# Kernel optimization log

Hardware: AMD Instinct MI355X
Metric: run time of the kernel (lower is better)

Reference implementation:

```python
import jax, jax.numpy as jnp
import numpy as np

N_NODES = 100000
N_EDGES = 3200000
N_GRAPHS = 2048
D_IN = 128
D_H = 128
D_OUT = 2
BN_EPS = 1e-5


def setup_inputs() -> dict:
    key = jax.random.key(0)
    ks = jax.random.split(key, 24)
    x = jax.random.normal(ks[0], (N_NODES, D_IN), dtype=jnp.float32)
    edge_index = jax.random.randint(ks[1], (2, N_EDGES), 0, N_NODES, dtype=jnp.int64)
    batch = jnp.sort(jax.random.randint(ks[2], (N_NODES,), 0, N_GRAPHS, dtype=jnp.int64))

    def lin(k, din, dout):
        return jax.random.normal(k, (din, dout), dtype=jnp.float32) / np.sqrt(din)

    inp = {
        'x': x, 'edge_index': edge_index, 'batch': batch,
        'W1': lin(ks[3], D_IN, D_H), 'b1': jnp.zeros((D_H,), jnp.float32),
        'W2': lin(ks[4], D_H, D_H), 'b2': jnp.zeros((D_H,), jnp.float32),
        'W3': lin(ks[5], D_H, D_H), 'b3': jnp.zeros((D_H,), jnp.float32),
    }
    for i, kk in zip((1, 2, 3), (ks[6], ks[7], ks[8])):
        inp[f'bn{i}_g'] = 1.0 + 0.1 * jax.random.normal(jax.random.fold_in(kk, 0), (D_H,), jnp.float32)
        inp[f'bn{i}_b'] = 0.1 * jax.random.normal(jax.random.fold_in(kk, 1), (D_H,), jnp.float32)
        inp[f'bn{i}_m'] = 0.1 * jax.random.normal(jax.random.fold_in(kk, 2), (D_H,), jnp.float32)
        inp[f'bn{i}_v'] = 0.5 + jax.random.uniform(jax.random.fold_in(kk, 3), (D_H,), jnp.float32)
    inp['fc1_W'] = lin(ks[9], D_H, D_H)
    inp['fc1_b'] = jnp.zeros((D_H,), jnp.float32)
    inp['fc2_W'] = lin(ks[10], D_H, D_OUT)
    inp['fc2_b'] = jnp.zeros((D_OUT,), jnp.float32)
    return inp


def _gcn_conv(x, W, b, src, dst, dinv):
    # h = X W, then out[dst] += (dinv[src]*dinv[dst]) * h[src]  (self-loops already in src/dst)
    h = x @ W
    norm = dinv[src] * dinv[dst]  # [E+N]
    msg = h[src] * norm[:, None]  # [E+N, D]
    out = jax.ops.segment_sum(msg, dst, num_segments=N_NODES)
    return out + b


def _bn_eval(x, g, b, m, v):
    return (x - m) * (g * jax.lax.rsqrt(v + BN_EPS)) + b


def reference(x, edge_index, batch, W1, b1, W2, b2, W3, b3,
              bn1_g, bn1_b, bn1_m, bn1_v, bn2_g, bn2_b, bn2_m, bn2_v,
              bn3_g, bn3_b, bn3_m, bn3_v, fc1_W, fc1_b, fc2_W, fc2_b):
    loops = jnp.arange(N_NODES, dtype=edge_index.dtype)
    src = jnp.concatenate([edge_index[0], loops])
    dst = jnp.concatenate([edge_index[1], loops])
    deg = jax.ops.segment_sum(jnp.ones_like(dst, dtype=x.dtype), dst, num_segments=N_NODES)
    dinv = jnp.where(deg > 0, jax.lax.rsqrt(jnp.maximum(deg, 1.0)), 0.0)

    h = jax.nn.relu(_bn_eval(_gcn_conv(x, W1, b1, src, dst, dinv), bn1_g, bn1_b, bn1_m, bn1_v))
    h = jax.nn.relu(_bn_eval(_gcn_conv(h, W2, b2, src, dst, dinv), bn2_g, bn2_b, bn2_m, bn2_v))
    h = jax.nn.relu(_bn_eval(_gcn_conv(h, W3, b3, src, dst, dinv), bn3_g, bn3_b, bn3_m, bn3_v))

    # global mean pool over graphs
    sums = jax.ops.segment_sum(h, batch, num_segments=N_GRAPHS)
    cnts = jax.ops.segment_sum(jnp.ones((N_NODES,), h.dtype), batch, num_segments=N_GRAPHS)
    pooled = sums / jnp.maximum(cnts, 1.0)[:, None]  # [G, D_H]

    z = jax.nn.relu(pooled @ fc1_W + fc1_b)
    logits = z @ fc2_W + fc2_b
    return jax.nn.log_softmax(logits, axis=1)
```

## Files before the change

### kernel.cpp

```cpp
#include <hip/hip_runtime.h>
#include <stdint.h>

#define NN 100000
#define NE 3200000
#define NG 2048
#define DH 128
#define NBLK_SCAN 49

#define NBUK 196
#define BSH 9
#define BMASK 511
#define BUKCAP 18200
#define EPT 16
#define EPW 4096

typedef __attribute__((ext_vector_type(8))) short v8s;
typedef __attribute__((ext_vector_type(4))) float v4f;

__device__ __forceinline__ float bf2f(unsigned short u) {
  union { unsigned int i; float f; } v; v.i = ((unsigned int)u) << 16; return v.f;
}
__device__ __forceinline__ unsigned short f2bf(float f) {
  union { float f; unsigned int i; } v; v.f = f;
  unsigned int i = v.i;
  unsigned int r = (i + 0x7FFFu + ((i >> 16) & 1u)) >> 16;
  return (unsigned short)r;
}
__device__ __forceinline__ int eload(const void* p, long long i, int is64) {
  return is64 ? (int)((const long long*)p)[i] : ((const int*)p)[i];
}
__device__ __forceinline__ float pload(const void* p, int i, int isbf) {
  return isbf ? bf2f(((const unsigned short*)p)[i]) : ((const float*)p)[i];
}
__device__ __forceinline__ void upadd(unsigned int w, float& lo, float& hi) {
  union { unsigned int u; float f; } a, b;
  a.u = w << 16; b.u = w & 0xffff0000u;
  lo += a.f; hi += b.f;
}

constexpr size_t al(size_t x) { return (x + 255) & ~size_t(255); }
constexpr size_t OFF_FLAGS = 0;
constexpr size_t OFF_DINV  = 256;
constexpr size_t OFF_ROWP  = al(OFF_DINV + 4ull * NN);
constexpr size_t OFF_GSTART= al(OFF_ROWP + 4ull * (NN + 1));
constexpr size_t OFF_BCUR  = al(OFF_GSTART + 4ull * (NG + 1));
constexpr size_t OFF_BSUM  = al(OFF_BCUR + 1024);
constexpr size_t OFF_BPRE  = al(OFF_BSUM + 256);
constexpr size_t OFF_WT    = al(OFF_BPRE + 256);
constexpr size_t OFF_FC1W  = al(OFF_WT + 2ull * 3 * 16384);
constexpr size_t OFF_FC2W  = al(OFF_FC1W + 4ull * 16384);
constexpr size_t OFF_PVEC  = al(OFF_FC2W + 4ull * 256);
constexpr size_t OFF_AC    = al(OFF_PVEC + 4ull * 17 * 128);
constexpr size_t OFF_COL   = al(OFF_AC + 4ull * 768);
constexpr size_t OFF_H     = al(OFF_COL + 4ull * NE);
constexpr size_t OFF_Y     = al(OFF_H + 2ull * NN * 128);
constexpr size_t WS_NEED   = OFF_Y + 2ull * NN * 128;
constexpr size_t OFF_REC   = OFF_H;
constexpr size_t OFF_DEG   = WS_NEED - 4ull * NN;

__global__ __launch_bounds__(256) void zero_k(int* p, int n) {
  int i = blockIdx.x * 256 + threadIdx.x;
  if (i < n) p[i] = 0;
}

__global__ __launch_bounds__(256) void probe_k(const void* edge, const void* batch,
                                               const void* x, int* flags) {
  __shared__ int cnt_e, cnt_b, cnt_f;
  int t = threadIdx.x;
  if (t == 0) { cnt_e = 0; cnt_b = 0; cnt_f = 0; }
  __syncthreads();
  int le = 0, lb = 0, lf = 0;
  for (int i = t; i < 512; i += 256) {
    uint2 p = ((const uint2*)edge)[i + 64];
    if (p.y != 0) le++;
  }
  for (int i = t; i < 512; i += 256) {
    uint2 p = ((const uint2*)batch)[50000 - 512 + i];
    if (p.y != 0) lb++;
  }
  for (int i = t; i < 4096; i += 256) {
    unsigned short u = ((const unsigned short*)x)[i];
    int e = (u >> 7) & 0xFF;
    if (e >= 0x90) lf++;
  }
  atomicAdd(&cnt_e, le); atomicAdd(&cnt_b, lb); atomicAdd(&cnt_f, lf);
  __syncthreads();
  if (t == 0) {
    flags[0] = (cnt_e == 0);
    flags[1] = (cnt_b == 0);
    flags[2] = (cnt_f < 16);
    flags[3] = 1;
  }
}

struct Ptrs { const void* p[22]; };

__global__ __launch_bounds__(256) void norm_param_k(Ptrs ptrs, const int* flags,
    unsigned short* Wt, float* fc1W, float* fc2W, float* pvec) {
  int isbf = flags[2];
  int idx = blockIdx.x * 256 + threadIdx.x;
  if (idx < 3 * 16384) {
    int l = idx / 16384, rem = idx % 16384;
    int c = rem >> 7, k = rem & 127;
    const void* W = ptrs.p[2 * l];
    Wt[l * 16384 + c * DH + k] = f2bf(pload(W, k * DH + c, isbf));
  } else if (idx < 4 * 16384) {
    int jj = idx - 3 * 16384;
    fc1W[jj] = pload(ptrs.p[18], jj, isbf);
  } else if (idx < 4 * 16384 + 256) {
    int jj = idx - 4 * 16384;
    fc2W[jj] = pload(ptrs.p[20], jj, isbf);
  } else if (idx < 4 * 16384 + 256 + 17 * 128) {
    int jj = idx - (4 * 16384 + 256);
    int slot = jj >> 7, e = jj & 127;
    int pi = (slot < 3) ? (1 + 2 * slot) : (slot < 15) ? (slot + 3) : (slot == 15 ? 19 : 21);
    if (slot == 16 && e >= 2) return;
    pvec[slot * 128 + e] = pload(ptrs.p[pi], e, isbf);
  }
}

__global__ __launch_bounds__(256) void prep_k(const float* pvec, float* AC) {
  int idx = blockIdx.x * 256 + threadIdx.x;
  if (idx >= 384) return;
  int l = idx >> 7, d = idx & 127;
  float b  = pvec[l * 128 + d];
  float g  = pvec[(3 + 4 * l) * 128 + d];
  float bb = pvec[(4 + 4 * l) * 128 + d];
  float m  = pvec[(5 + 4 * l) * 128 + d];
  float v  = pvec[(6 + 4 * l) * 128 + d];
  float s = g * rsqrtf(v + 1e-5f);
  AC[l * 256 + d] = s;
  AC[l * 256 + 128 + d] = (b - m) * s + bb;
}

__global__ __launch_bounds__(256) void partition_k(const void* edge, const int* flags,
    int* bcur, unsigned long long* recs) {
  __shared__ int lhist[NBUK];
  __shared__ int lbase[NBUK];
  __shared__ int lrank[NBUK];
  int t = threadIdx.x;
  for (int b = t; b < NBUK; b += 256) { lhist[b] = 0; lrank[b] = 0; }
  __syncthreads();
  long long e0 = (long long)blockIdx.x * EPW;
  int f = flags[0];
  int sv[EPT], dv[EPT];
  #pragma unroll
  for (int k = 0; k < EPT; ++k) {
    long long e = e0 + k * 256 + t;
    int s = 0, d = -1;
    if (e < NE) {
      s = eload(edge, e, f);
      d = eload(edge, NE + e, f);
      if ((unsigned)s >= NN || (unsigned)d >= NN) d = -1;
    }
    sv[k] = s; dv[k] = d;
    if (d >= 0) atomicAdd(&lhist[d >> BSH], 1);
  }
  __syncthreads();
  for (int b = t; b < NBUK; b += 256)
    lbase[b] = atomicAdd(&bcur[b], lhist[b]);
  __syncthreads();
  #pragma unroll
  for (int k = 0; k < EPT; ++k) {
    int d = dv[k];
    if (d >= 0) {
      int b = d >> BSH;
      int r = atomicAdd(&lrank[b], 1);
      int pos = lbase[b] + r;
      if (pos < BUKCAP)
        recs[(size_t)b * BUKCAP + pos] =
            ((unsigned long long)(unsigned)d << 32) | (unsigned)sv[k];
    }
  }
}

__global__ __launch_bounds__(256) void bucket_deg_k(const unsigned long long* recs,
    const int* bcur, int* deg) {
  __shared__ int lh[1 << BSH];
  int b = blockIdx.x, t = threadIdx.x;
  for (int i = t; i < (1 << BSH); i += 256) lh[i] = 0;
  __syncthreads();
  int cnt = bcur[b]; if (cnt > BUKCAP) cnt = BUKCAP;
  const unsigned long long* rb = recs + (size_t)b * BUKCAP;
  for (int i = t; i < cnt; i += 256) {
    int d = (int)(rb[i] >> 32);
    atomicAdd(&lh[d & BMASK], 1);
  }
  __syncthreads();
  int base = b << BSH;
  for (int i = t; i < (1 << BSH); i += 256) {
    int n = base + i;
    if (n < NN) deg[n] = lh[i];
  }
}

__global__ __launch_bounds__(256) void debucket_k(const unsigned long long* recs,
    const int* bcur, const int* rowp, int* colv) {
  __shared__ int lrk[1 << BSH];
  int b = blockIdx.x, t = threadIdx.x;
  for (int i = t; i < (1 << BSH); i += 256) lrk[i] = 0;
  __syncthreads();
  int cnt = bcur[b]; if (cnt > BUKCAP) cnt = BUKCAP;
  const unsigned long long* rb = recs + (size_t)b * BUKCAP;
  for (int i = t; i < cnt; i += 256) {
    unsigned long long rec = rb[i];
    int d = (int)(rec >> 32);
    int s = (int)(rec & 0xffffffffu);
    int r = atomicAdd(&lrk[d & BMASK], 1);
    colv[rowp[d] + r] = s;
  }
}

__global__ __launch_bounds__(256) void dinv_k(const int* deg, float* dinv) {
  int n = blockIdx.x * 256 + threadIdx.x;
  if (n < NN) dinv[n] = rsqrtf((float)(deg[n] + 1));
}

__global__ __launch_bounds__(256) void scan1_k(const int* deg, int* bsum) {
  __shared__ int ts[256];
  int t = threadIdx.x;
  int base = blockIdx.x * 2048 + t * 8;
  int s = 0;
  #pragma unroll
  for (int k = 0; k < 8; ++k) { int i = base + k; s += (i < NN) ? deg[i] : 0; }
  ts[t] = s; __syncthreads();
  for (int off = 128; off > 0; off >>= 1) {
    if (t < off) ts[t] += ts[t + off];
    __syncthreads();
  }
  if (t == 0) bsum[blockIdx.x] = ts[0];
}

__global__ void scan2_k(const int* bsum, int* bpre, int* rowp) {
  if (threadIdx.x == 0 && blockIdx.x == 0) {
    int run = 0;
    for (int b = 0; b < NBLK_SCAN; ++b) { bpre[b] = run; run += bsum[b]; }
    rowp[NN] = run;
  }
}

__global__ __launch_bounds__(256) void scan3_k(const int* deg, const int* bpre, int* rowp) {
  __shared__ int ts[256];
  int t = threadIdx.x;
  int base = blockIdx.x * 2048 + t * 8;
  int v[8]; int s = 0;
  #pragma unroll
  for (int k = 0; k < 8; ++k) { int i = base + k; v[k] = (i < NN) ? deg[i] : 0; s += v[k]; }
  ts[t] = s; __syncthreads();
  for (int off = 1; off < 256; off <<= 1) {
    int x = (t >= off) ? ts[t - off] : 0;
    __syncthreads();
    ts[t] += x;
    __syncthreads();
  }
  int pre = bpre[blockIdx.x] + ts[t] - s;
  #pragma unroll
  for (int k = 0; k < 8; ++k) { int i = base + k; if (i < NN) rowp[i] = pre; pre += v[k]; }
}

__global__ __launch_bounds__(256) void gbound_k(const void* batch, const int* flags,
                                                int* gstart) {
  int i = blockIdx.x * 256 + threadIdx.x;
  if (i >= NN) return;
  int f = flags[1];
  int b = eload(batch, i, f);
  if ((unsigned)b >= NG) b = NG - 1;
  int bp = -1;
  if (i > 0) {
    bp = eload(batch, i - 1, f);
    if ((unsigned)bp >= NG) bp = NG - 1;
  }
  for (int g = bp + 1; g <= b; ++g) gstart[g] = i;
  if (i == NN - 1) {
    for (int g = b + 1; g <= NG; ++g) gstart[g] = NN;
  }
}

__global__ __launch_bounds__(256) void gemm_k(const void* A, const int* flagp,
    const unsigned short* Wt, const float* dinv, unsigned short* H) {
  const int wave = threadIdx.x >> 6;
  const int lane = threadIdx.x & 63;
  const int rowbase = blockIdx.x * 64 + wave * 16;
  const int r = lane & 15;
  const int g = lane >> 4;
  const int isb = flagp[0];
  int arow = rowbase + r;
  int arowc = (arow < NN) ? arow : 0;

  v8s a[4];
  if (isb) {
    const uint4* Ab = (const uint4*)A;
    #pragma unroll
    for (int ks = 0; ks < 4; ++ks) {
      union { uint4 u; v8s v; } t;
      t.u = Ab[(arowc * DH + ks * 32 + g * 8) >> 3];
      a[ks] = t.v;
    }
  } else {
    const float4* Af = (const float4*)A;
    #pragma unroll
    for (int ks = 0; ks < 4; ++ks) {
      int bi = (arowc * DH + ks * 32 + g * 8) >> 2;
      float4 f0 = Af[bi], f1 = Af[bi + 1];
      v8s t;
      t[0]=(short)f2bf(f0.x); t[1]=(short)f2bf(f0.y); t[2]=(short)f2bf(f0.z); t[3]=(short)f2bf(f0.w);
      t[4]=(short)f2bf(f1.x); t[5]=(short)f2bf(f1.y); t[6]=(short)f2bf(f1.z); t[7]=(short)f2bf(f1.w);
      a[ks] = t;
    }
  }
  int orow0 = rowbase + g * 4;
  float dv[4];
  #pragma unroll
  for (int j = 0; j < 4; ++j) {
    int orow = orow0 + j;
    dv[j] = dinv[(orow < NN) ? orow : 0];
  }
  const uint4* Wb = (const uint4*)Wt;
  #pragma unroll
  for (int ct = 0; ct < 8; ++ct) {
    v4f acc = {0.f, 0.f, 0.f, 0.f};
    #pragma unroll
    for (int ks = 0; ks < 4; ++ks) {
      union { uint4 u; v8s v; } t;
      t.u = Wb[((ct * 16 + r) * DH + ks * 32 + g * 8) >> 3];
      acc = __builtin_amdgcn_mfma_f32_16x16x32_bf16(a[ks], t.v, acc, 0, 0, 0);
    }
    #pragma unroll
    for (int j = 0; j < 4; ++j) {
      int orow = orow0 + j;
      if (orow < NN) H[orow * DH + ct * 16 + r] = f2bf(acc[j] * dv[j]);
    }
  }
}

__global__ __launch_bounds__(256) void agg_k(const unsigned short* H, const int* rowp,
    const int* colv, const float* dinv, const float* Avec, const float* Cvec,
    unsigned short* Y) {
  int n = blockIdx.x * 4 + (threadIdx.x >> 6);
  if (n >= NN) return;
  int lane = threadIdx.x & 63;
  int q = lane >> 4;
  int c16 = lane & 15;
  const uint4* H4 = (const uint4*)H;
  float a0=0.f,a1=0.f,a2=0.f,a3=0.f,a4=0.f,a5=0.f,a6=0.f,a7=0.f;
  int beg = rowp[n], end = rowp[n + 1];
  int j = beg;
  for (; j + 8 <= end; j += 8) {
    int s0 = colv[j + q];
    int s1 = colv[j + 4 + q];
    uint4 v0 = H4[s0 * 16 + c16];
    uint4 v1 = H4[s1 * 16 + c16];
    upadd(v0.x, a0, a1); upadd(v0.y, a2, a3);
    upadd(v0.z, a4, a5); upadd(v0.w, a6, a7);
    upadd(v1.x, a0, a1); upadd(v1.y, a2, a3);
    upadd(v1.z, a4, a5); upadd(v1.w, a6, a7);
  }
  for (; j + 4 <= end; j += 4) {
    int s0 = colv[j + q];
    uint4 v0 = H4[s0 * 16 + c16];
    upadd(v0.x, a0, a1); upadd(v0.y, a2, a3);
    upadd(v0.z, a4, a5); upadd(v0.w, a6, a7);
  }
  {
    int e = j + q;
    if (e < end) {
      int s0 = colv[e];
      uint4 v0 = H4[s0 * 16 + c16];
      upadd(v0.x, a0, a1); upadd(v0.y, a2, a3);
      upadd(v0.z, a4, a5); upadd(v0.w, a6, a7);
    }
  }
  #pragma unroll
  for (int m = 16; m <= 32; m <<= 1) {
    a0 += __shfl_xor(a0, m); a1 += __shfl_xor(a1, m);
    a2 += __shfl_xor(a2, m); a3 += __shfl_xor(a3, m);
    a4 += __shfl_xor(a4, m); a5 += __shfl_xor(a5, m);
    a6 += __shfl_xor(a6, m); a7 += __shfl_xor(a7, m);
  }
  if (q == 0) {
    uint4 sv = H4[n * 16 + c16];
    upadd(sv.x, a0, a1); upadd(sv.y, a2, a3);
    upadd(sv.z, a4, a5); upadd(sv.w, a6, a7);
    float dvn = dinv[n];
    int f0 = c16 * 8;
    float y0 = fmaxf(a0 * dvn * Avec[f0+0] + Cvec[f0+0], 0.f);
    float y1 = fmaxf(a1 * dvn * Avec[f0+1] + Cvec[f0+1], 0.f);
    float y2 = fmaxf(a2 * dvn * Avec[f0+2] + Cvec[f0+2], 0.f);
    float y3 = fmaxf(a3 * dvn * Avec[f0+3] + Cvec[f0+3], 0.f);
    float y4 = fmaxf(a4 * dvn * Avec[f0+4] + Cvec[f0+4], 0.f);
    float y5 = fmaxf(a5 * dvn * Avec[f0+5] + Cvec[f0+5], 0.f);
    float y6 = fmaxf(a6 * dvn * Avec[f0+6] + Cvec[f0+6], 0.f);
    float y7 = fmaxf(a7 * dvn * Avec[f0+7] + Cvec[f0+7], 0.f);
    uint4 o;
    o.x = (unsigned int)f2bf(y0) | ((unsigned int)f2bf(y1) << 16);
    o.y = (unsigned int)f2bf(y2) | ((unsigned int)f2bf(y3) << 16);
    o.z = (unsigned int)f2bf(y4) | ((unsigned int)f2bf(y5) << 16);
    o.w = (unsigned int)f2bf(y6) | ((unsigned int)f2bf(y7) << 16);
    ((uint4*)Y)[n * 16 + c16] = o;
  }
}

__global__ __launch_bounds__(256) void pool_k(const unsigned short* Y, const int* gstart,
                                              float* pooled) {
  int g = blockIdx.x * 4 + (threadIdx.x >> 6);
  if (g >= NG) return;
  int lane = threadIdx.x & 63;
  const unsigned int* Yu = (const unsigned int*)Y;
  int beg = gstart[g], end = gstart[g + 1];
  int cnt = end - beg;
  float a0 = 0.f, a1 = 0.f;
  for (int i = beg; i < end; ++i) {
    unsigned int v = Yu[i * 64 + lane];
    a0 += bf2f((unsigned short)v); a1 += bf2f((unsigned short)(v >> 16));
  }
  float inv = 1.f / fmaxf((float)cnt, 1.f);
  pooled[g * DH + lane * 2]     = a0 * inv;
  pooled[g * DH + lane * 2 + 1] = a1 * inv;
}

__global__ __launch_bounds__(256) void fc1_k(const float* pooled, const float* fc1W,
                                             const float* pvec, float* Z) {
  int idx = blockIdx.x * 256 + threadIdx.x;
  int g = idx >> 7, c = idx & 127;
  if (g >= NG) return;
  float acc = 0.f;
  const float* pr = pooled + g * DH;
  #pragma unroll 8
  for (int k = 0; k < DH; ++k) acc += pr[k] * fc1W[k * DH + c];
  acc += pvec[15 * 128 + c];
  Z[g * DH + c] = fmaxf(acc, 0.f);
}

__global__ __launch_bounds__(256) void fc2_k(const float* Z, const float* fc2W,
                                             const float* pvec, float* out) {
  int g = blockIdx.x * 256 + threadIdx.x;
  if (g >= NG) return;
  float l0 = pvec[16 * 128 + 0], l1 = pvec[16 * 128 + 1];
  const float* zr = Z + g * DH;
  #pragma unroll 8
  for (int k = 0; k < DH; ++k) { float z = zr[k]; l0 += z * fc2W[k * 2]; l1 += z * fc2W[k * 2 + 1]; }
  float m = fmaxf(l0, l1);
  float lse = m + logf(expf(l0 - m) + expf(l1 - m));
  out[g * 2]     = l0 - lse;
  out[g * 2 + 1] = l1 - lse;
}

extern "C" void kernel_launch(void* const* d_in, const int* in_sizes, int n_in,
                              void* d_out, int out_size, void* d_ws, size_t ws_size,
                              hipStream_t stream) {
  char* ws = (char*)d_ws;
  int*   flags  = (int*)(ws + OFF_FLAGS);
  float* dinvp  = (float*)(ws + OFF_DINV);
  int*   rowp   = (int*)(ws + OFF_ROWP);
  int*   gstart = (int*)(ws + OFF_GSTART);
  int*   bcur   = (int*)(ws + OFF_BCUR);
  int*   bsum   = (int*)(ws + OFF_BSUM);
  int*   bpre   = (int*)(ws + OFF_BPRE);
  unsigned short* Wt  = (unsigned short*)(ws + OFF_WT);
  float* fc1W   = (float*)(ws + OFF_FC1W);
  float* fc2W   = (float*)(ws + OFF_FC2W);
  float* pvec   = (float*)(ws + OFF_PVEC);
  float* AC     = (float*)(ws + OFF_AC);
  int*   colv   = (int*)(ws + OFF_COL);
  unsigned short* Hbuf = (unsigned short*)(ws + OFF_H);
  unsigned short* Ybuf = (unsigned short*)(ws + OFF_Y);
  unsigned long long* recs = (unsigned long long*)(ws + OFF_REC);
  int*   deg    = (int*)(ws + OFF_DEG);
  float* pooled = (float*)(ws + OFF_COL);
  float* Z      = (float*)(ws + OFF_COL + 4ull * NG * DH);

  const void* x     = d_in[0];
  const void* edge  = d_in[1];
  const void* batch = d_in[2];

  zero_k<<<1, 256, 0, stream>>>(bcur, 256);
  probe_k<<<1, 256, 0, stream>>>(edge, batch, x, flags);

  Ptrs P;
  for (int i = 0; i < 22; ++i) P.p[i] = d_in[3 + i];
  norm_param_k<<<266, 256, 0, stream>>>(P, flags, Wt, fc1W, fc2W, pvec);
  prep_k<<<2, 256, 0, stream>>>(pvec, AC);

  partition_k<<<(NE + EPW - 1) / EPW, 256, 0, stream>>>(edge, flags, bcur, recs);
  bucket_deg_k<<<NBUK, 256, 0, stream>>>(recs, bcur, deg);
  gbound_k<<<(NN + 255) / 256, 256, 0, stream>>>(batch, flags, gstart);
  dinv_k<<<(NN + 255) / 256, 256, 0, stream>>>(deg, dinvp);
  scan1_k<<<NBLK_SCAN, 256, 0, stream>>>(deg, bsum);
  scan2_k<<<1, 64, 0, stream>>>(bsum, bpre, rowp);
  scan3_k<<<NBLK_SCAN, 256, 0, stream>>>(deg, bpre, rowp);
  debucket_k<<<NBUK, 256, 0, stream>>>(recs, bcur, rowp, colv);

  const int GB = (NN + 63) / 64;
  gemm_k<<<GB, 256, 0, stream>>>(x, flags + 2, Wt, dinvp, Hbuf);
  agg_k<<<NN / 4, 256, 0, stream>>>(Hbuf, rowp, colv, dinvp, AC, AC + 128, Ybuf);
  gemm_k<<<GB, 256, 0, stream>>>(Ybuf, flags + 3, Wt + 16384, dinvp, Hbuf);
  agg_k<<<NN / 4, 256, 0, stream>>>(Hbuf, rowp, colv, dinvp, AC + 256, AC + 384, Ybuf);
  gemm_k<<<GB, 256, 0, stream>>>(Ybuf, flags + 3, Wt + 32768, dinvp, Hbuf);
  agg_k<<<NN / 4, 256, 0, stream>>>(Hbuf, rowp, colv, dinvp, AC + 512, AC + 640, Ybuf);

  pool_k<<<NG / 4, 256, 0, stream>>>(Ybuf, gstart, pooled);
  fc1_k<<<(NG * DH) / 256, 256, 0, stream>>>(pooled, fc1W, pvec, Z);
  fc2_k<<<(NG + 255) / 256, 256, 0, stream>>>(Z, fc2W, pvec, (float*)d_out);
}
```

Before: 595.2 us.

## Sub-bucket edges by source range to sort CSR columns; unroll aggregation with packed float2

```diff
diff --git a/kernel.cpp b/kernel.cpp
--- a/kernel.cpp
+++ b/kernel.cpp
@@ -10,12 +10,16 @@
 #define NBUK 196
 #define BSH 9
 #define BMASK 511
-#define BUKCAP 18200
+#define NBUK_S 7
+#define SSH 14
+#define NBUKT (NBUK_S * NBUK)
+#define BUKCAP 3100
 #define EPT 16
 #define EPW 4096
 
 typedef __attribute__((ext_vector_type(8))) short v8s;
 typedef __attribute__((ext_vector_type(4))) float v4f;
+typedef __attribute__((ext_vector_type(2))) float f2;
 
 __device__ __forceinline__ float bf2f(unsigned short u) {
   union { unsigned int i; float f; } v; v.i = ((unsigned int)u) << 16; return v.f;
@@ -32,10 +36,11 @@
 __device__ __forceinline__ float pload(const void* p, int i, int isbf) {
   return isbf ? bf2f(((const unsigned short*)p)[i]) : ((const float*)p)[i];
 }
-__device__ __forceinline__ void upadd(unsigned int w, float& lo, float& hi) {
+__device__ __forceinline__ void upadd2(unsigned int w, f2& acc) {
   union { unsigned int u; float f; } a, b;
   a.u = w << 16; b.u = w & 0xffff0000u;
-  lo += a.f; hi += b.f;
+  f2 u; u.x = a.f; u.y = b.f;
+  acc += u;
 }
 
 constexpr size_t al(size_t x) { return (x + 255) & ~size_t(255); }
@@ -44,7 +49,7 @@
 constexpr size_t OFF_ROWP  = al(OFF_DINV + 4ull * NN);
 constexpr size_t OFF_GSTART= al(OFF_ROWP + 4ull * (NN + 1));
 constexpr size_t OFF_BCUR  = al(OFF_GSTART + 4ull * (NG + 1));
-constexpr size_t OFF_BSUM  = al(OFF_BCUR + 1024);
+constexpr size_t OFF_BSUM  = al(OFF_BCUR + 4ull * 1408);
 constexpr size_t OFF_BPRE  = al(OFF_BSUM + 256);
 constexpr size_t OFF_WT    = al(OFF_BPRE + 256);
 constexpr size_t OFF_FC1W  = al(OFF_WT + 2ull * 3 * 16384);
@@ -135,11 +140,11 @@
 
 __global__ __launch_bounds__(256) void partition_k(const void* edge, const int* flags,
     int* bcur, unsigned long long* recs) {
-  __shared__ int lhist[NBUK];
-  __shared__ int lbase[NBUK];
-  __shared__ int lrank[NBUK];
+  __shared__ int lhist[NBUKT];
+  __shared__ int lbase[NBUKT];
+  __shared__ int lrank[NBUKT];
   int t = threadIdx.x;
-  for (int b = t; b < NBUK; b += 256) { lhist[b] = 0; lrank[b] = 0; }
+  for (int b = t; b < NBUKT; b += 256) { lhist[b] = 0; lrank[b] = 0; }
   __syncthreads();
   long long e0 = (long long)blockIdx.x * EPW;
   int f = flags[0];
@@ -154,17 +159,17 @@
       if ((unsigned)s >= NN || (unsigned)d >= NN) d = -1;
     }
     sv[k] = s; dv[k] = d;
-    if (d >= 0) atomicAdd(&lhist[d >> BSH], 1);
-  }
-  __syncthreads();
-  for (int b = t; b < NBUK; b += 256)
+    if (d >= 0) atomicAdd(&lhist[(s >> SSH) * NBUK + (d >> BSH)], 1);
+  }
+  __syncthreads();
+  for (int b = t; b < NBUKT; b += 256)
     lbase[b] = atomicAdd(&bcur[b], lhist[b]);
   __syncthreads();
   #pragma unroll
   for (int k = 0; k < EPT; ++k) {
     int d = dv[k];
     if (d >= 0) {
-      int b = d >> BSH;
+      int b = (sv[k] >> SSH) * NBUK + (d >> BSH);
       int r = atomicAdd(&lrank[b], 1);
       int pos = lbase[b] + r;
       if (pos < BUKCAP)
@@ -180,11 +185,14 @@
   int b = blockIdx.x, t = threadIdx.x;
   for (int i = t; i < (1 << BSH); i += 256) lh[i] = 0;
   __syncthreads();
-  int cnt = bcur[b]; if (cnt > BUKCAP) cnt = BUKCAP;
-  const unsigned long long* rb = recs + (size_t)b * BUKCAP;
-  for (int i = t; i < cnt; i += 256) {
-    int d = (int)(rb[i] >> 32);
-    atomicAdd(&lh[d & BMASK], 1);
+  for (int g = 0; g < NBUK_S; ++g) {
+    int bb = g * NBUK + b;
+    int cnt = bcur[bb]; if (cnt > BUKCAP) cnt = BUKCAP;
+    const unsigned long long* rb = recs + (size_t)bb * BUKCAP;
+    for (int i = t; i < cnt; i += 256) {
+      int d = (int)(rb[i] >> 32);
+      atomicAdd(&lh[d & BMASK], 1);
+    }
   }
   __syncthreads();
   int base = b << BSH;
@@ -200,14 +208,18 @@
   int b = blockIdx.x, t = threadIdx.x;
   for (int i = t; i < (1 << BSH); i += 256) lrk[i] = 0;
   __syncthreads();
-  int cnt = bcur[b]; if (cnt > BUKCAP) cnt = BUKCAP;
-  const unsigned long long* rb = recs + (size_t)b * BUKCAP;
-  for (int i = t; i < cnt; i += 256) {
-    unsigned long long rec = rb[i];
-    int d = (int)(rec >> 32);
-    int s = (int)(rec & 0xffffffffu);
-    int r = atomicAdd(&lrk[d & BMASK], 1);
-    colv[rowp[d] + r] = s;
+  for (int g = 0; g < NBUK_S; ++g) {
+    int bb = g * NBUK + b;
+    int cnt = bcur[bb]; if (cnt > BUKCAP) cnt = BUKCAP;
+    const unsigned long long* rb = recs + (size_t)bb * BUKCAP;
+    for (int i = t; i < cnt; i += 256) {
+      unsigned long long rec = rb[i];
+      int d = (int)(rec >> 32);
+      int s = (int)(rec & 0xffffffffu);
+      int r = atomicAdd(&lrk[d & BMASK], 1);
+      colv[rowp[d] + r] = s;
+    }
+    __syncthreads();
   }
 }
 
@@ -341,56 +353,54 @@
   int lane = threadIdx.x & 63;
   int q = lane >> 4;
   int c16 = lane & 15;
-  const uint4* H4 = (const uint4*)H;
-  float a0=0.f,a1=0.f,a2=0.f,a3=0.f,a4=0.f,a5=0.f,a6=0.f,a7=0.f;
+  const uint4* Hc = (const uint4*)H + c16;
+  f2 a01 = {0.f, 0.f}, a23 = {0.f, 0.f}, a45 = {0.f, 0.f}, a67 = {0.f, 0.f};
   int beg = rowp[n], end = rowp[n + 1];
   int j = beg;
-  for (; j + 8 <= end; j += 8) {
+  #define ACC4(v) do { upadd2((v).x, a01); upadd2((v).y, a23); \
+                       upadd2((v).z, a45); upadd2((v).w, a67); } while (0)
+  for (; j + 16 <= end; j += 16) {
     int s0 = colv[j + q];
     int s1 = colv[j + 4 + q];
-    uint4 v0 = H4[s0 * 16 + c16];
-    uint4 v1 = H4[s1 * 16 + c16];
-    upadd(v0.x, a0, a1); upadd(v0.y, a2, a3);
-    upadd(v0.z, a4, a5); upadd(v0.w, a6, a7);
-    upadd(v1.x, a0, a1); upadd(v1.y, a2, a3);
-    upadd(v1.z, a4, a5); upadd(v1.w, a6, a7);
+    int s2 = colv[j + 8 + q];
+    int s3 = colv[j + 12 + q];
+    uint4 v0 = Hc[s0 * 16];
+    uint4 v1 = Hc[s1 * 16];
+    uint4 v2 = Hc[s2 * 16];
+    uint4 v3 = Hc[s3 * 16];
+    ACC4(v0); ACC4(v1); ACC4(v2); ACC4(v3);
   }
   for (; j + 4 <= end; j += 4) {
     int s0 = colv[j + q];
-    uint4 v0 = H4[s0 * 16 + c16];
-    upadd(v0.x, a0, a1); upadd(v0.y, a2, a3);
-    upadd(v0.z, a4, a5); upadd(v0.w, a6, a7);
-  }
-  {
-    int e = j + q;
-    if (e < end) {
-      int s0 = colv[e];
-      uint4 v0 = H4[s0 * 16 + c16];
-      upadd(v0.x, a0, a1); upadd(v0.y, a2, a3);
-      upadd(v0.z, a4, a5); upadd(v0.w, a6, a7);
-    }
-  }
+    uint4 v0 = Hc[s0 * 16];
+    ACC4(v0);
+  }
+  if (j + q < end) {
+    uint4 v0 = Hc[colv[j + q] * 16];
+    ACC4(v0);
+  }
+  #undef ACC4
   #pragma unroll
   for (int m = 16; m <= 32; m <<= 1) {
-    a0 += __shfl_xor(a0, m); a1 += __shfl_xor(a1, m);
-    a2 += __shfl_xor(a2, m); a3 += __shfl_xor(a3, m);
-    a4 += __shfl_xor(a4, m); a5 += __shfl_xor(a5, m);
-    a6 += __shfl_xor(a6, m); a7 += __shfl_xor(a7, m);
+    a01.x += __shfl_xor(a01.x, m); a01.y += __shfl_xor(a01.y, m);
+    a23.x += __shfl_xor(a23.x, m); a23.y += __shfl_xor(a23.y, m);
+    a45.x += __shfl_xor(a45.x, m); a45.y += __shfl_xor(a45.y, m);
+    a67.x += __shfl_xor(a67.x, m); a67.y += __shfl_xor(a67.y, m);
   }
   if (q == 0) {
-    uint4 sv = H4[n * 16 + c16];
-    upadd(sv.x, a0, a1); upadd(sv.y, a2, a3);
-    upadd(sv.z, a4, a5); upadd(sv.w, a6, a7);
+    uint4 sv = Hc[n * 16];
+    upadd2(sv.x, a01); upadd2(sv.y, a23);
+    upadd2(sv.z, a45); upadd2(sv.w, a67);
     float dvn = dinv[n];
     int f0 = c16 * 8;
-    float y0 = fmaxf(a0 * dvn * Avec[f0+0] + Cvec[f0+0], 0.f);
-    float y1 = fmaxf(a1 * dvn * Avec[f0+1] + Cvec[f0+1], 0.f);
-    float y2 = fmaxf(a2 * dvn * Avec[f0+2] + Cvec[f0+2], 0.f);
-    float y3 = fmaxf(a3 * dvn * Avec[f0+3] + Cvec[f0+3], 0.f);
-    float y4 = fmaxf(a4 * dvn * Avec[f0+4] + Cvec[f0+4], 0.f);
-    float y5 = fmaxf(a5 * dvn * Avec[f0+5] + Cvec[f0+5], 0.f);
-    float y6 = fmaxf(a6 * dvn * Avec[f0+6] + Cvec[f0+6], 0.f);
-    float y7 = fmaxf(a7 * dvn * Avec[f0+7] + Cvec[f0+7], 0.f);
+    float y0 = fmaxf(a01.x * dvn * Avec[f0+0] + Cvec[f0+0], 0.f);
+    float y1 = fmaxf(a01.y * dvn * Avec[f0+1] + Cvec[f0+1], 0.f);
+    float y2 = fmaxf(a23.x * dvn * Avec[f0+2] + Cvec[f0+2], 0.f);
+    float y3 = fmaxf(a23.y * dvn * Avec[f0+3] + Cvec[f0+3], 0.f);
+    float y4 = fmaxf(a45.x * dvn * Avec[f0+4] + Cvec[f0+4], 0.f);
+    float y5 = fmaxf(a45.y * dvn * Avec[f0+5] + Cvec[f0+5], 0.f);
+    float y6 = fmaxf(a67.x * dvn * Avec[f0+6] + Cvec[f0+6], 0.f);
+    float y7 = fmaxf(a67.y * dvn * Avec[f0+7] + Cvec[f0+7], 0.f);
     uint4 o;
     o.x = (unsigned int)f2bf(y0) | ((unsigned int)f2bf(y1) << 16);
     o.y = (unsigned int)f2bf(y2) | ((unsigned int)f2bf(y3) << 16);
@@ -473,7 +483,7 @@
   const void* edge  = d_in[1];
   const void* batch = d_in[2];
 
-  zero_k<<<1, 256, 0, stream>>>(bcur, 256);
+  zero_k<<<6, 256, 0, stream>>>(bcur, NBUKT);
   probe_k<<<1, 256, 0, stream>>>(edge, batch, x, flags);
 
   Ptrs P;
```

After: 613.6 us. +3.1%, slower.
